# Kernel tuning notes

Measured on AMD Instinct MI355X. Metric: run time of the kernel, lower is better.

Reference implementation:

```python
import jax, jax.numpy as jnp
import numpy as np

CONTEXT_SIZE = 256  # hardcoded in source; scale = context_size**-0.5, not head_size
EMBED_DIM = 384
HEAD_SIZE = 64
BATCH = 512
SEQ = 256


def setup_inputs() -> dict:
    key = jax.random.key(0)
    ks = jax.random.split(key, 7)
    s = 1.0 / np.sqrt(EMBED_DIM)
    return {
        "x": jax.random.normal(ks[0], (BATCH, SEQ, EMBED_DIM), jnp.float32),
        "Wq": jax.random.uniform(ks[1], (EMBED_DIM, HEAD_SIZE), jnp.float32, -s, s),
        "bq": jax.random.uniform(ks[2], (HEAD_SIZE,), jnp.float32, -s, s),
        "Wk": jax.random.uniform(ks[3], (EMBED_DIM, HEAD_SIZE), jnp.float32, -s, s),
        "bk": jax.random.uniform(ks[4], (HEAD_SIZE,), jnp.float32, -s, s),
        "Wv": jax.random.uniform(ks[5], (EMBED_DIM, HEAD_SIZE), jnp.float32, -s, s),
        "bv": jax.random.uniform(ks[6], (HEAD_SIZE,), jnp.float32, -s, s),
    }


def reference(x, Wq, bq, Wk, bk, Wv, bv):
    # x: [B, T, D]
    T = x.shape[1]
    q = x @ Wq + bq          # [B, T, H]
    k = x @ Wk + bk          # [B, T, H]
    v = x @ Wv + bv          # [B, T, H]
    scale = CONTEXT_SIZE ** (-0.5)  # faithful: source scales by context_size, not head_size
    scores = jnp.einsum("bth,bsh->bts", q, k) * scale  # [B, T, T]
    causal = jnp.tril(jnp.ones((T, T), dtype=bool))
    scores = jnp.where(causal, scores, -jnp.inf)
    attn = jax.nn.softmax(scores, axis=-1)
    # dropout omitted (eval mode / deterministic reference)
    return jnp.einsum("bts,bsh->bth", attn, v)  # [B, T, H]
```

## Files before the change

### kernel.cpp

```cpp
#include <hip/hip_runtime.h>
#include <hip/hip_bf16.h>
#include <stdint.h>

#define B_ 512
#define T_ 256
#define D_ 384
#define H_ 64

typedef __attribute__((ext_vector_type(8))) short bf16x8;
typedef __attribute__((ext_vector_type(4))) float f32x4;
typedef __attribute__((ext_vector_type(16))) float f32x16;

__device__ __forceinline__ unsigned short f2bf(float f) {
  union { float f; unsigned int u; } a; a.f = f;
  unsigned int r = (a.u + 0x7FFFu + ((a.u >> 16) & 1u)) >> 16;
  return (unsigned short)r;
}

__device__ __forceinline__ unsigned int pkbf(float lo, float hi) {
  unsigned int r;
  asm("v_cvt_pk_bf16_f32 %0, %1, %2" : "=v"(r) : "v"(lo), "v"(hi));
  return r;
}

__device__ __forceinline__ void gld16(const void* g, void* l) {
  __builtin_amdgcn_global_load_lds(
      (const __attribute__((address_space(1))) unsigned int*)g,
      (__attribute__((address_space(3))) unsigned int*)l, 16, 0, 0);
}

__global__ void prep_wt(const float* __restrict__ Wq, const float* __restrict__ Wk,
                        const float* __restrict__ Wv, unsigned short* __restrict__ wt) {
  int idx = blockIdx.x * 256 + threadIdx.x;
  if (idx >= 192 * 384) return;
  int n = idx / 384, k = idx - n * 384;
  int sel = n >> 6, c = n & 63;
  const float* W = (sel == 0) ? Wq : ((sel == 1) ? Wk : Wv);
  wt[idx] = f2bf(W[k * 64 + c]);
}

__global__ __launch_bounds__(512) void attn_fused(
    const float* __restrict__ x, const float* __restrict__ bq,
    const float* __restrict__ bk, const float* __restrict__ bv,
    const unsigned short* __restrict__ wt, float* __restrict__ out) {
  extern __shared__ char smem[];
  const int tid = threadIdx.x;
  const int b = blockIdx.x;
  const int wv = tid >> 6, lane = tid & 63;
  const int lo4 = lane & 15, hi4 = lane >> 4;
  const int lo5 = lane & 31, hi5 = lane >> 5;

  const float* xb = x + (size_t)b * T_ * D_;

  f32x4 acc[2][12];
#pragma unroll
  for (int rt = 0; rt < 2; ++rt)
#pragma unroll
    for (int ct = 0; ct < 12; ++ct) acc[rt][ct] = (f32x4)0.0f;

  auto issue_tile = [&](int t) {
    char* bx = smem + (t & 1) * 32768;
    char* bw = smem + 65536 + (t & 1) * 12288;
#pragma unroll
    for (int i = 0; i < 4; ++i) {
      int ub = 256 * wv + 64 * i;
      int u = ub + lane;
      int row = u >> 3;
      int c = (u & 7) ^ (row & 7);
      gld16((const char*)xb + (size_t)row * 1536 + 128 * t + 16 * c, bx + 16 * ub);
    }
    if (wv < 6) {
#pragma unroll
      for (int i = 0; i < 2; ++i) {
        int ub = 128 * wv + 64 * i;
        int u = ub + lane;
        int n = u >> 2;
        int c = (u & 3) ^ (n & 3);
        gld16((const char*)wt + (size_t)n * 768 + 64 * t + 16 * c, bw + 16 * ub);
      }
    }
  };

  auto compute_tile = [&](int t) {
    const char* bx = smem + (t & 1) * 32768;
    const char* bw = smem + 65536 + (t & 1) * 12288;
    bf16x8 afr[2];
#pragma unroll
    for (int rt = 0; rt < 2; ++rt) {
      int row = 32 * wv + 16 * rt + lo4;
      int u0 = 8 * row + ((2 * hi4) ^ (row & 7));
      int u1 = 8 * row + ((2 * hi4 + 1) ^ (row & 7));
      float4 f0 = *reinterpret_cast<const float4*>(bx + 16 * u0);
      float4 f1 = *reinterpret_cast<const float4*>(bx + 16 * u1);
      union { bf16x8 v; unsigned int w[4]; } A;
      A.w[0] = pkbf(f0.x, f0.y); A.w[1] = pkbf(f0.z, f0.w);
      A.w[2] = pkbf(f1.x, f1.y); A.w[3] = pkbf(f1.z, f1.w);
      afr[rt] = A.v;
    }
#pragma unroll
    for (int ct = 0; ct < 12; ++ct) {
      int n = 16 * ct + lo4;
      int uB = 4 * n + (hi4 ^ (n & 3));
      bf16x8 bwf = *reinterpret_cast<const bf16x8*>(bw + 16 * uB);
      acc[0][ct] = __builtin_amdgcn_mfma_f32_16x16x32_bf16(afr[0], bwf, acc[0][ct], 0, 0, 0);
      acc[1][ct] = __builtin_amdgcn_mfma_f32_16x16x32_bf16(afr[1], bwf, acc[1][ct], 0, 0, 0);
    }
  };

  issue_tile(0);
  issue_tile(1);
#pragma unroll 1
  for (int t = 0; t < 12; ++t) {
    if (t < 11) {
      if (wv < 6) asm volatile("s_waitcnt vmcnt(6)" ::: "memory");
      else        asm volatile("s_waitcnt vmcnt(4)" ::: "memory");
    } else {
      asm volatile("s_waitcnt vmcnt(0)" ::: "memory");
    }
    __builtin_amdgcn_sched_barrier(0);
    __builtin_amdgcn_s_barrier();
    __builtin_amdgcn_sched_barrier(0);
    compute_tile(t);
    __builtin_amdgcn_sched_barrier(0);
    __builtin_amdgcn_s_barrier();
    __builtin_amdgcn_sched_barrier(0);
    if (t < 10) issue_tile(t + 2);
  }

#pragma unroll
  for (int ct = 0; ct < 12; ++ct) {
    int n = 16 * ct + lo4;
    float bias = (ct < 4) ? bq[n] : ((ct < 8) ? bk[n - 64] : bv[n - 128]);
#pragma unroll
    for (int rt = 0; rt < 2; ++rt) {
      int rowb = 32 * wv + 16 * rt + 4 * hi4;
#pragma unroll
      for (int r = 0; r < 4; ++r) {
        int row = rowb + r;
        unsigned short v = f2bf(acc[rt][ct][r] + bias);
        if (ct < 4) {
          int h = n;
          *reinterpret_cast<unsigned short*>(smem + row * 128 + ((2 * h) ^ ((row & 7) << 4))) = v;
        } else if (ct < 8) {
          int h = n - 64;
          *reinterpret_cast<unsigned short*>(smem + 32768 + row * 128 + ((2 * h) ^ ((row & 7) << 4))) = v;
        } else {
          int h = n - 128;
          *reinterpret_cast<unsigned short*>(smem + 65536 + h * 512 + ((2 * row) ^ ((h & 7) << 4))) = v;
        }
      }
    }
  }
  __syncthreads();

  const float cexp = 0.09016844005555897f;

  bf16x8 qf[4];
  {
    int row = 32 * wv + lo5;
#pragma unroll
    for (int s = 0; s < 4; ++s)
      qf[s] = *reinterpret_cast<const bf16x8*>(
          smem + row * 128 + (((32 * s + 16 * hi5)) ^ ((row & 7) << 4)));
  }

  f32x16 o0 = (f32x16)0.0f, o1 = (f32x16)0.0f;
  float lsum = 0.0f;

  for (int kb = 0; kb <= wv; ++kb) {
    f32x16 st = (f32x16)0.0f;
    {
      int row = 32 * kb + lo5;
#pragma unroll
      for (int s = 0; s < 4; ++s) {
        bf16x8 kf = *reinterpret_cast<const bf16x8*>(
            smem + 32768 + row * 128 + (((32 * s + 16 * hi5)) ^ ((row & 7) << 4)));
        st = __builtin_amdgcn_mfma_f32_32x32x16_bf16(kf, qf[s], st, 0, 0, 0);
      }
    }
    float p[16];
#pragma unroll
    for (int r = 0; r < 16; ++r) {
      float e = exp2f(cexp * st[r]);
      if (kb == wv) {
        int keyl = (r & 3) + 8 * (r >> 2) + 4 * hi5;
        if (keyl > lo5) e = 0.0f;
      }
      p[r] = e;
      lsum += e;
    }

    union { bf16x8 v; unsigned int w[4]; } A0, A1;
    {
      unsigned int X0 = pkbf(p[0], p[1]),  X1 = pkbf(p[2], p[3]);
      unsigned int Y0 = pkbf(p[4], p[5]),  Y1 = pkbf(p[6], p[7]);
      unsigned int X0p = (unsigned int)__shfl_xor((int)X0, 32);
      unsigned int X1p = (unsigned int)__shfl_xor((int)X1, 32);
      unsigned int Y0p = (unsigned int)__shfl_xor((int)Y0, 32);
      unsigned int Y1p = (unsigned int)__shfl_xor((int)Y1, 32);
      A0.w[0] = hi5 ? Y0p : X0;
      A0.w[1] = hi5 ? Y1p : X1;
      A0.w[2] = hi5 ? Y0  : X0p;
      A0.w[3] = hi5 ? Y1  : X1p;
      unsigned int Z0 = pkbf(p[8], p[9]),   Z1 = pkbf(p[10], p[11]);
      unsigned int W0 = pkbf(p[12], p[13]), W1 = pkbf(p[14], p[15]);
      unsigned int Z0p = (unsigned int)__shfl_xor((int)Z0, 32);
      unsigned int Z1p = (unsigned int)__shfl_xor((int)Z1, 32);
      unsigned int W0p = (unsigned int)__shfl_xor((int)W0, 32);
      unsigned int W1p = (unsigned int)__shfl_xor((int)W1, 32);
      A1.w[0] = hi5 ? W0p : Z0;
      A1.w[1] = hi5 ? W1p : Z1;
      A1.w[2] = hi5 ? W0  : Z0p;
      A1.w[3] = hi5 ? W1  : Z1p;
    }
#pragma unroll
    for (int s2 = 0; s2 < 2; ++s2) {
      bf16x8 pa = s2 ? A1.v : A0.v;
      int kk = 32 * kb + 16 * s2 + 8 * hi5;
#pragma unroll
      for (int ht = 0; ht < 2; ++ht) {
        int h = 32 * ht + lo5;
        bf16x8 vf = *reinterpret_cast<const bf16x8*>(
            smem + 65536 + h * 512 + (((2 * kk)) ^ ((h & 7) << 4)));
        if (ht == 0) o0 = __builtin_amdgcn_mfma_f32_32x32x16_bf16(pa, vf, o0, 0, 0, 0);
        else         o1 = __builtin_amdgcn_mfma_f32_32x32x16_bf16(pa, vf, o1, 0, 0, 0);
      }
    }
  }

  lsum += __shfl_xor(lsum, 32);
  float inv = 1.0f / lsum;
  float* ob = out + (size_t)b * T_ * H_;
#pragma unroll
  for (int r = 0; r < 16; ++r) {
    int ridx = (r & 3) + 8 * (r >> 2) + 4 * hi5;
    float invr = __shfl(inv, ridx);
    int row = 32 * wv + ridx;
    ob[row * H_ + lo5]      = o0[r] * invr;
    ob[row * H_ + 32 + lo5] = o1[r] * invr;
  }
}

extern "C" void kernel_launch(void* const* d_in, const int* in_sizes, int n_in,
                              void* d_out, int out_size, void* d_ws, size_t ws_size,
                              hipStream_t stream) {
  const float* x  = (const float*)d_in[0];
  const float* Wq = (const float*)d_in[1];
  const float* bq = (const float*)d_in[2];
  const float* Wk = (const float*)d_in[3];
  const float* bk = (const float*)d_in[4];
  const float* Wv = (const float*)d_in[5];
  const float* bv = (const float*)d_in[6];
  unsigned short* wt = (unsigned short*)d_ws;
  float* out = (float*)d_out;

  prep_wt<<<288, 256, 0, stream>>>(Wq, Wk, Wv, wt);
  attn_fused<<<B_, 512, 98304, stream>>>(x, bq, bk, bv, wt, out);
}
```

Measured before the change: 66.07 us.

## Switch projection GEMM to fp16 MFMA with 4-stage, half-size K tiles

```diff
diff --git a/kernel.cpp b/kernel.cpp
--- a/kernel.cpp
+++ b/kernel.cpp
@@ -1,5 +1,6 @@
 #include <hip/hip_runtime.h>
 #include <hip/hip_bf16.h>
+#include <hip/hip_fp16.h>
 #include <stdint.h>
 
 #define B_ 512
@@ -8,6 +9,8 @@
 #define H_ 64
 
 typedef __attribute__((ext_vector_type(8))) short bf16x8;
+typedef __attribute__((ext_vector_type(4))) _Float16 f16x4;
+typedef __attribute__((ext_vector_type(2))) __fp16 fp16x2;
 typedef __attribute__((ext_vector_type(4))) float f32x4;
 typedef __attribute__((ext_vector_type(16))) float f32x16;
 
@@ -21,6 +24,13 @@
   unsigned int r;
   asm("v_cvt_pk_bf16_f32 %0, %1, %2" : "=v"(r) : "v"(lo), "v"(hi));
   return r;
+}
+
+__device__ __forceinline__ f16x4 pk4(float a, float b, float c, float d) {
+  union { fp16x2 h[2]; f16x4 v; } U;
+  U.h[0] = __builtin_amdgcn_cvt_pkrtz(a, b);
+  U.h[1] = __builtin_amdgcn_cvt_pkrtz(c, d);
+  return U.v;
 }
 
 __device__ __forceinline__ void gld16(const void* g, void* l) {
@@ -36,7 +46,8 @@
   int n = idx / 384, k = idx - n * 384;
   int sel = n >> 6, c = n & 63;
   const float* W = (sel == 0) ? Wq : ((sel == 1) ? Wk : Wv);
-  wt[idx] = f2bf(W[k * 64 + c]);
+  __half h = __float2half(W[k * 64 + c]);
+  wt[idx] = *reinterpret_cast<const unsigned short*>(&h);
 }
 
 __global__ __launch_bounds__(512) void attn_fused(
@@ -59,63 +70,59 @@
     for (int ct = 0; ct < 12; ++ct) acc[rt][ct] = (f32x4)0.0f;
 
   auto issue_tile = [&](int t) {
-    char* bx = smem + (t & 1) * 32768;
-    char* bw = smem + 65536 + (t & 1) * 12288;
-#pragma unroll
-    for (int i = 0; i < 4; ++i) {
-      int ub = 256 * wv + 64 * i;
+    char* bx = smem + (t & 3) * 16384;
+    char* bw = smem + 65536 + (t & 3) * 6144;
+#pragma unroll
+    for (int i = 0; i < 2; ++i) {
+      int ub = 128 * wv + 64 * i;
       int u = ub + lane;
-      int row = u >> 3;
-      int c = (u & 7) ^ (row & 7);
-      gld16((const char*)xb + (size_t)row * 1536 + 128 * t + 16 * c, bx + 16 * ub);
+      int row = u >> 2;
+      int c = (u & 3) ^ ((row >> 1) & 3);
+      gld16((const char*)xb + (size_t)row * 1536 + 64 * t + 16 * c, bx + 16 * ub);
     }
     if (wv < 6) {
-#pragma unroll
-      for (int i = 0; i < 2; ++i) {
-        int ub = 128 * wv + 64 * i;
-        int u = ub + lane;
-        int n = u >> 2;
-        int c = (u & 3) ^ (n & 3);
-        gld16((const char*)wt + (size_t)n * 768 + 64 * t + 16 * c, bw + 16 * ub);
-      }
+      int ub = 64 * wv;
+      int u = ub + lane;
+      int n = u >> 1;
+      int c = (u & 1) ^ ((n >> 2) & 1);
+      gld16((const char*)wt + (size_t)n * 768 + 32 * t + 16 * c, bw + 16 * ub);
     }
   };
 
   auto compute_tile = [&](int t) {
-    const char* bx = smem + (t & 1) * 32768;
-    const char* bw = smem + 65536 + (t & 1) * 12288;
-    bf16x8 afr[2];
+    const char* bx = smem + (t & 3) * 16384;
+    const char* bw = smem + 65536 + (t & 3) * 6144;
+    f16x4 afr[2];
 #pragma unroll
     for (int rt = 0; rt < 2; ++rt) {
       int row = 32 * wv + 16 * rt + lo4;
-      int u0 = 8 * row + ((2 * hi4) ^ (row & 7));
-      int u1 = 8 * row + ((2 * hi4 + 1) ^ (row & 7));
-      float4 f0 = *reinterpret_cast<const float4*>(bx + 16 * u0);
-      float4 f1 = *reinterpret_cast<const float4*>(bx + 16 * u1);
-      union { bf16x8 v; unsigned int w[4]; } A;
-      A.w[0] = pkbf(f0.x, f0.y); A.w[1] = pkbf(f0.z, f0.w);
-      A.w[2] = pkbf(f1.x, f1.y); A.w[3] = pkbf(f1.z, f1.w);
-      afr[rt] = A.v;
+      int u = 4 * row + (hi4 ^ ((row >> 1) & 3));
+      float4 f0 = *reinterpret_cast<const float4*>(bx + 16 * u);
+      afr[rt] = pk4(f0.x, f0.y, f0.z, f0.w);
     }
 #pragma unroll
     for (int ct = 0; ct < 12; ++ct) {
       int n = 16 * ct + lo4;
-      int uB = 4 * n + (hi4 ^ (n & 3));
-      bf16x8 bwf = *reinterpret_cast<const bf16x8*>(bw + 16 * uB);
-      acc[0][ct] = __builtin_amdgcn_mfma_f32_16x16x32_bf16(afr[0], bwf, acc[0][ct], 0, 0, 0);
-      acc[1][ct] = __builtin_amdgcn_mfma_f32_16x16x32_bf16(afr[1], bwf, acc[1][ct], 0, 0, 0);
+      int off = 32 * n + 16 * ((hi4 >> 1) ^ ((n >> 2) & 1)) + 8 * (hi4 & 1);
+      f16x4 bwf = *reinterpret_cast<const f16x4*>(bw + off);
+      acc[0][ct] = __builtin_amdgcn_mfma_f32_16x16x16f16(afr[0], bwf, acc[0][ct], 0, 0, 0);
+      acc[1][ct] = __builtin_amdgcn_mfma_f32_16x16x16f16(afr[1], bwf, acc[1][ct], 0, 0, 0);
     }
   };
 
-  issue_tile(0);
-  issue_tile(1);
+  issue_tile(0); issue_tile(1); issue_tile(2); issue_tile(3);
 #pragma unroll 1
-  for (int t = 0; t < 12; ++t) {
-    if (t < 11) {
-      if (wv < 6) asm volatile("s_waitcnt vmcnt(6)" ::: "memory");
-      else        asm volatile("s_waitcnt vmcnt(4)" ::: "memory");
+  for (int t = 0; t < 24; ++t) {
+    if (wv < 6) {
+      if (t <= 20)      asm volatile("s_waitcnt vmcnt(9)" ::: "memory");
+      else if (t == 21) asm volatile("s_waitcnt vmcnt(6)" ::: "memory");
+      else if (t == 22) asm volatile("s_waitcnt vmcnt(3)" ::: "memory");
+      else              asm volatile("s_waitcnt vmcnt(0)" ::: "memory");
     } else {
-      asm volatile("s_waitcnt vmcnt(0)" ::: "memory");
+      if (t <= 20)      asm volatile("s_waitcnt vmcnt(6)" ::: "memory");
+      else if (t == 21) asm volatile("s_waitcnt vmcnt(4)" ::: "memory");
+      else if (t == 22) asm volatile("s_waitcnt vmcnt(2)" ::: "memory");
+      else              asm volatile("s_waitcnt vmcnt(0)" ::: "memory");
     }
     __builtin_amdgcn_sched_barrier(0);
     __builtin_amdgcn_s_barrier();
@@ -124,7 +131,7 @@
     __builtin_amdgcn_sched_barrier(0);
     __builtin_amdgcn_s_barrier();
     __builtin_amdgcn_sched_barrier(0);
-    if (t < 10) issue_tile(t + 2);
+    if (t < 20) issue_tile(t + 4);
   }
 
 #pragma unroll
```

Result: slower. 82.13 us (+24.3%).
